# Kernel tuning notes

Hardware: AMD Instinct MI355X
Metric: run time of the kernel (lower is better)

The kernel has to match this reference:

```python
import jax, jax.numpy as jnp
import numpy as np

DN = ('NCDHW', 'DHWIO', 'NCDHW')


def _w(key, cin, cout):
    # kernel_size=3 in 3D, Minkowski-style fan-in scaling, no bias
    scale = 1.0 / np.sqrt(cin * 27)
    return jax.random.normal(key, (3, 3, 3, cin, cout), dtype=jnp.float32) * scale


def setup_inputs() -> dict:
    key = jax.random.key(0)
    ks = jax.random.split(key, 7)
    x = jax.random.normal(ks[0], (1, 1024, 4, 4, 4), dtype=jnp.float32)
    chans = [(1024, 512), (512, 256), (256, 128), (128, 64), (64, 32), (32, 1)]
    ws = {f'w{i+1}': _w(ks[i + 1], ci, co) for i, (ci, co) in enumerate(chans)}
    return {'x': x, **ws}


def _ct(x, w, stride):
    # conv-transpose, kernel 3, SAME padding: stride 2 doubles resolution,
    # stride 1 preserves it (dense analog of Minkowski generative transpose conv)
    return jax.lax.conv_transpose(x, w, strides=(stride, stride, stride),
                                  padding='SAME', dimension_numbers=DN)


def reference(x, w1, w2, w3, w4, w5, w6):
    h = jax.nn.relu(_ct(x, w1, 2))   # 1024 -> 512, 4^3 -> 8^3
    h = jax.nn.relu(_ct(h, w2, 1))   # 512 -> 256
    h = jax.nn.relu(_ct(h, w3, 2))   # 256 -> 128, 8^3 -> 16^3
    h = jax.nn.relu(_ct(h, w4, 1))   # 128 -> 64
    h = jax.nn.relu(_ct(h, w5, 2))   # 64 -> 32, 16^3 -> 32^3
    return _ct(h, w6, 1)             # 32 -> 1, no final ReLU
```

## Files before the change

kernel.cpp:

```cpp
#include <hip/hip_runtime.h>

typedef _Float16 half8 __attribute__((ext_vector_type(8)));
typedef _Float16 half4v __attribute__((ext_vector_type(4)));
typedef float floatx4 __attribute__((ext_vector_type(4)));


__global__ __launch_bounds__(256) void pad_x_k(const float* __restrict__ X,
                                               _Float16* __restrict__ P) {
  int idx = blockIdx.x * 256 + threadIdx.x;
  if (idx >= 125 * 1024) return;
  int c = idx & 1023;
  int r = idx >> 10;
  int px = r % 5, py = (r / 5) % 5, pz = r / 25;
  float v = 0.f;
  if (px >= 1 && py >= 1 && pz >= 1)
    v = X[c * 64 + (pz - 1) * 16 + (py - 1) * 4 + (px - 1)];
  P[idx] = (_Float16)v;
}

template <int S, int PS, int C, int RELU>
__global__ __launch_bounds__(256) void pad_k(const float* __restrict__ I,
                                             _Float16* __restrict__ P) {
  constexpr int TOT = PS * PS * PS * C;
  int idx = blockIdx.x * 256 + threadIdx.x;
  if (idx >= TOT) return;
  int c = idx % C;
  int r = idx / C;
  int px = r % PS;
  int ry = r / PS;
  int py = ry % PS, pz = ry / PS;
  int sx = px - 1, sy = py - 1, sz = pz - 1;
  float v = 0.f;
  if (sx >= 0 && sx < S && sy >= 0 && sy < S && sz >= 0 && sz < S) {
    v = I[(size_t)((sz * S + sy) * S + sx) * C + c];
    if (RELU) v = fmaxf(v, 0.f);
  }
  P[idx] = (_Float16)v;
}

template <int CICHUNK, int CIN, int COUT, int NTILE, int STRIDE2, int SOUTU,
          int TZ, int PS, int STORE_MODE>
__global__ __launch_bounds__(256) void conv_mfma_k(
    const _Float16* __restrict__ P, const float* __restrict__ W,
    void* __restrict__ Optr) {
  constexpr int M = TZ * 16;
  constexpr int MTZ = SOUTU / TZ;
  constexpr int MTXY = SOUTU / 4;
  constexpr int MT3 = MTZ * MTXY * MTXY;
  constexpr int KB = 32;
  constexpr int KP = 40;
  constexpr int KBI = CICHUNK / KB;
  constexpr int S = STRIDE2 ? 2 * SOUTU : SOUTU;
  constexpr int BJ = (NTILE == 64) ? 8 : 4;

  __shared__ __align__(16) _Float16 As[M][KP];
  __shared__ __align__(16) _Float16 Bs[NTILE][KP];

  int bx = blockIdx.x;
  int cls = 0;
  if (STRIDE2) { cls = bx / MT3; bx -= cls * MT3; }
  const int clz = (cls >> 2) & 1, cly = (cls >> 1) & 1, clx = cls & 1;
  const int u0z = (bx / (MTXY * MTXY)) * TZ;
  const int u0y = ((bx / MTXY) % MTXY) * 4;
  const int u0x = (bx % MTXY) * 4;
  const int n_base = blockIdx.y * NTILE;
  const int ci_base = blockIdx.z * CICHUNK;

  const int t = threadIdx.x;
  const int lane = t & 63;
  const int wave = t >> 6;

  const int skq = t & 3;
  const int sp = t >> 2;
  const int spx = sp & 3, spy = (sp >> 2) & 3, spz = sp >> 4;
  const int aoffsp = ((spz * PS + spy) * PS + spx) * CIN + skq * 8;
  const int aoffsp2 = (((spz + 4) * PS + spy) * PS + spx) * CIN + skq * 8;

  const int nB = t & (NTILE - 1);
  const int k0B = (t / NTILE) * BJ;

  const int m0w = (NTILE == 64) ? (wave >> 1) * 32 : wave * 32;
  const int n0w = (NTILE == 64) ? (wave & 1) * 32 : 0;
  const int fr = lane & 15;
  const int fq = lane >> 4;

  const int cz = STRIDE2 ? (clz ? 1 : 2) : 3;
  const int cy = STRIDE2 ? (cly ? 1 : 2) : 3;
  const int cx = STRIDE2 ? (clx ? 1 : 2) : 3;
  const int ctaps = cz * cy * cx;
  const int NIT = ctaps * KBI;
  const int shx = STRIDE2 ? (clx ? 0 : 1) : 0;
  const int shy = STRIDE2 ? (cly ? 0 : 1) : 0;

  floatx4 acc[2][2];
#pragma unroll
  for (int i = 0; i < 2; i++)
#pragma unroll
    for (int j = 0; j < 2; j++) acc[i][j] = {0.f, 0.f, 0.f, 0.f};

  half8 raA = {}, raB = {}, raA2 = {}, raB2 = {};
  float bwv[BJ] = {}, bwv2[BJ] = {};

  auto load_it = [&](int it, half8& A0, half8& A1, float* BW) {
    int tap, kb;
    if (KBI == 1) { tap = it; kb = 0; }
    else { tap = it / KBI; kb = it - tap * KBI; }
    int iz, iy, ix;
    if (STRIDE2) {
      const int shyx = shx + shy;
      iz = tap >> shyx;
      int rem = tap - (iz << shyx);
      iy = rem >> shx;
      ix = rem - (iy << shx);
    } else {
      iz = tap / 9;
      int rem = tap - iz * 9;
      iy = rem / 3;
      ix = rem - iy * 3;
    }
    const int toz = STRIDE2 ? (clz ? 1 : iz) : iz;
    const int wz  = STRIDE2 ? (clz ? 1 : 2 * iz) : iz;
    const int toy = STRIDE2 ? (cly ? 1 : iy) : iy;
    const int wy  = STRIDE2 ? (cly ? 1 : 2 * iy) : iy;
    const int tox = STRIDE2 ? (clx ? 1 : ix) : ix;
    const int wx  = STRIDE2 ? (clx ? 1 : 2 * ix) : ix;
    const int kofs = ci_base + kb * KB;
    const size_t pbase =
        (size_t)(((u0z + toz) * PS + (u0y + toy)) * PS + (u0x + tox)) * CIN +
        kofs;
    A0 = *(const half8*)(P + pbase + aoffsp);
    if (M == 128) A1 = *(const half8*)(P + pbase + aoffsp2);
    const int wtap = (wz * 3 + wy) * 3 + wx;
    const float* wb =
        W + ((size_t)wtap * CIN + kofs + k0B) * COUT + n_base + nB;
#pragma unroll
    for (int j = 0; j < BJ; j++) BW[j] = wb[(size_t)j * COUT];
  };

  load_it(0, raA, raB, bwv);

  for (int it = 0; it < NIT; ++it) {
    *(half8*)&As[sp][skq * 8] = raA;
    if (M == 128) *(half8*)&As[sp + 64][skq * 8] = raB;
    {
      half4v h0;
#pragma unroll
      for (int j = 0; j < 4; j++) h0[j] = (_Float16)bwv[j];
      *(half4v*)&Bs[nB][k0B] = h0;
      if (BJ == 8) {
        half4v h1;
#pragma unroll
        for (int j = 0; j < 4; j++) h1[j] = (_Float16)bwv[4 + j];
        *(half4v*)&Bs[nB][k0B + 4] = h1;
      }
    }
    __syncthreads();
    if (it + 1 < NIT) load_it(it + 1, raA2, raB2, bwv2);
    half8 a0 = *(const half8*)&As[m0w + fr][fq * 8];
    half8 a1 = *(const half8*)&As[m0w + 16 + fr][fq * 8];
    half8 b0 = *(const half8*)&Bs[n0w + fr][fq * 8];
    half8 b1 = *(const half8*)&Bs[n0w + 16 + fr][fq * 8];
    acc[0][0] = __builtin_amdgcn_mfma_f32_16x16x32_f16(a0, b0, acc[0][0], 0, 0, 0);
    acc[0][1] = __builtin_amdgcn_mfma_f32_16x16x32_f16(a0, b1, acc[0][1], 0, 0, 0);
    acc[1][0] = __builtin_amdgcn_mfma_f32_16x16x32_f16(a1, b0, acc[1][0], 0, 0, 0);
    acc[1][1] = __builtin_amdgcn_mfma_f32_16x16x32_f16(a1, b1, acc[1][1], 0, 0, 0);
    __syncthreads();
    raA = raA2;
    raB = raB2;
#pragma unroll
    for (int j = 0; j < BJ; j++) bwv[j] = bwv2[j];
  }

#pragma unroll
  for (int i = 0; i < 2; i++) {
#pragma unroll
    for (int r = 0; r < 4; r++) {
      const int m = m0w + i * 16 + fq * 4 + r;
      const int mz = m >> 4, my = (m >> 2) & 3, mx = m & 3;
      int oz, oy, ox;
      if (STRIDE2) {
        oz = 2 * (u0z + mz) + clz;
        oy = 2 * (u0y + my) + cly;
        ox = 2 * (u0x + mx) + clx;
      } else {
        oz = u0z + mz;
        oy = u0y + my;
        ox = u0x + mx;
      }
      if (STORE_MODE == 2) {
        _Float16* o = (_Float16*)Optr +
            (size_t)(((oz + 1) * (S + 2) + (oy + 1)) * (S + 2) + (ox + 1)) *
                COUT + n_base + n0w;
#pragma unroll
        for (int j = 0; j < 2; j++)
          o[j * 16 + fr] = (_Float16)fmaxf(acc[i][j][r], 0.f);
      } else {
        float* o = (float*)Optr +
            (size_t)((oz * S + oy) * S + ox) * COUT + n_base + n0w;
#pragma unroll
        for (int j = 0; j < 2; j++) {
          if (STORE_MODE == 1) atomicAdd(o + j * 16 + fr, acc[i][j][r]);
          else o[j * 16 + fr] = acc[i][j][r];
        }
      }
    }
  }
}

__global__ __launch_bounds__(256) void conv6_k(const _Float16* __restrict__ P,
                                               const float* __restrict__ W6,
                                               float* __restrict__ O) {
  __shared__ __align__(16) float w[864];
  for (int i = threadIdx.x; i < 864; i += 256) w[i] = W6[i];
  __syncthreads();
  int idx = blockIdx.x * 256 + threadIdx.x;
  int x = idx & 31, y = (idx >> 5) & 31, z = idx >> 10;
  float a = 0.f;
  for (int dz = 0; dz < 3; dz++)
    for (int dy = 0; dy < 3; dy++)
      for (int dx = 0; dx < 3; dx++) {
        const _Float16* p =
            P + (size_t)(((z + dz) * 34 + (y + dy)) * 34 + (x + dx)) * 32;
        const float* ww = &w[((dz * 3 + dy) * 3 + dx) * 32];
#pragma unroll
        for (int c = 0; c < 32; c += 8) {
          half8 pv = *(const half8*)&p[c];
#pragma unroll
          for (int u = 0; u < 8; u++) a += (float)pv[u] * ww[c + u];
        }
      }
  O[idx] = a;
}

extern "C" void kernel_launch(void* const* d_in, const int* in_sizes, int n_in,
                              void* d_out, int out_size, void* d_ws,
                              size_t ws_size, hipStream_t stream) {
  const float* x  = (const float*)d_in[0];
  const float* w1 = (const float*)d_in[1];
  const float* w2 = (const float*)d_in[2];
  const float* w3 = (const float*)d_in[3];
  const float* w4 = (const float*)d_in[4];
  const float* w5 = (const float*)d_in[5];
  const float* w6 = (const float*)d_in[6];
  float* out = (float*)d_out;

  float* O1 = (float*)d_ws;
  float* O2 = O1 + 262144;
  float* O3 = O2 + 131072;
  float* O4 = O3 + 524288;
  _Float16* P6 = (_Float16*)(O4 + 262144);
  _Float16* P1 = P6 + 1257728;
  _Float16* P2 = P1 + 128000;
  _Float16* P3 = P2 + 512000;
  _Float16* P4 = P3 + 186624;
  _Float16* P5 = P4 + 746496;

  hipMemsetAsync(d_ws, 0, 1179648 * sizeof(float) + 1257728 * sizeof(_Float16),
                 stream);

  pad_x_k<<<500, 256, 0, stream>>>(x, P1);
  conv_mfma_k<128, 1024, 512, 64, 1, 4, 4, 5, 1>
      <<<dim3(8, 8, 8), 256, 0, stream>>>(P1, w1, O1);
  pad_k<8, 10, 512, 1><<<2000, 256, 0, stream>>>(O1, P2);
  conv_mfma_k<32, 512, 256, 64, 0, 8, 4, 10, 1>
      <<<dim3(8, 4, 16), 256, 0, stream>>>(P2, w2, O2);
  pad_k<8, 9, 256, 1><<<729, 256, 0, stream>>>(O2, P3);
  conv_mfma_k<64, 256, 128, 64, 1, 8, 4, 9, 1>
      <<<dim3(64, 2, 4), 256, 0, stream>>>(P3, w3, O3);
  pad_k<16, 18, 128, 1><<<2916, 256, 0, stream>>>(O3, P4);
  conv_mfma_k<32, 128, 64, 64, 0, 16, 4, 18, 1>
      <<<dim3(64, 1, 4), 256, 0, stream>>>(P4, w4, O4);
  pad_k<16, 17, 64, 1><<<1229, 256, 0, stream>>>(O4, P5);
  conv_mfma_k<64, 64, 32, 32, 1, 16, 8, 17, 2>
      <<<dim3(256, 1, 1), 256, 0, stream>>>(P5, w5, P6);
  conv6_k<<<128, 256, 0, stream>>>(P6, w6, out);

  (void)in_sizes; (void)n_in; (void)out_size; (void)ws_size;
}
```

Measured before the change: 216.1 us.

## Fuse pad+ReLU into conv loads and split work across taps for parallelism

Removes the separate pad_k kernels: conv layers now read fp32 activations directly with bounds checks, apply ReLU and convert to fp16 in the load path. Adds per-tap parallel splitting (each block handles one tap for stride-2 layers or a group of 9 taps for stride-1) with atomic accumulation. Also adds M=128 tiles with 4-wave M layout. This cuts launches and intermediate traffic but increases atomic contention and redundant fp32 loads.

```diff
diff --git a/kernel.cpp b/kernel.cpp
--- a/kernel.cpp
+++ b/kernel.cpp
@@ -18,53 +18,79 @@
   P[idx] = (_Float16)v;
 }
 
-template <int S, int PS, int C, int RELU>
-__global__ __launch_bounds__(256) void pad_k(const float* __restrict__ I,
-                                             _Float16* __restrict__ P) {
-  constexpr int TOT = PS * PS * PS * C;
-  int idx = blockIdx.x * 256 + threadIdx.x;
-  if (idx >= TOT) return;
-  int c = idx % C;
-  int r = idx / C;
-  int px = r % PS;
-  int ry = r / PS;
-  int py = ry % PS, pz = ry / PS;
-  int sx = px - 1, sy = py - 1, sz = pz - 1;
-  float v = 0.f;
-  if (sx >= 0 && sx < S && sy >= 0 && sy < S && sz >= 0 && sz < S) {
-    v = I[(size_t)((sz * S + sy) * S + sx) * C + c];
-    if (RELU) v = fmaxf(v, 0.f);
-  }
-  P[idx] = (_Float16)v;
-}
-
-template <int CICHUNK, int CIN, int COUT, int NTILE, int STRIDE2, int SOUTU,
-          int TZ, int PS, int STORE_MODE>
+__device__ __forceinline__ half8 cvt_relu8(const float4& f0, const float4& f1) {
+  half8 h;
+  h[0] = (_Float16)fmaxf(f0.x, 0.f);
+  h[1] = (_Float16)fmaxf(f0.y, 0.f);
+  h[2] = (_Float16)fmaxf(f0.z, 0.f);
+  h[3] = (_Float16)fmaxf(f0.w, 0.f);
+  h[4] = (_Float16)fmaxf(f1.x, 0.f);
+  h[5] = (_Float16)fmaxf(f1.y, 0.f);
+  h[6] = (_Float16)fmaxf(f1.z, 0.f);
+  h[7] = (_Float16)fmaxf(f1.w, 0.f);
+  return h;
+}
+
+template <int CICHUNK, int CIN, int COUT, int NTILE, int TZ, int SOUTU,
+          int SMODE, int TAPG, int IN_MODE, int STORE_MODE>
 __global__ __launch_bounds__(256) void conv_mfma_k(
-    const _Float16* __restrict__ P, const float* __restrict__ W,
+    const void* __restrict__ Pin, const float* __restrict__ W,
     void* __restrict__ Optr) {
   constexpr int M = TZ * 16;
+  constexpr bool S2 = (SMODE != 0);
   constexpr int MTZ = SOUTU / TZ;
   constexpr int MTXY = SOUTU / 4;
   constexpr int MT3 = MTZ * MTXY * MTXY;
   constexpr int KB = 32;
   constexpr int KP = 40;
   constexpr int KBI = CICHUNK / KB;
-  constexpr int S = STRIDE2 ? 2 * SOUTU : SOUTU;
-  constexpr int BJ = (NTILE == 64) ? 8 : 4;
+  constexpr int NCI = CIN / CICHUNK;
+  constexpr int S = S2 ? 2 * SOUTU : SOUTU;
+  constexpr int WM = (M == 128) ? 4 : 2;
+  constexpr int NSUB = (WM == 4) ? (NTILE / 16) : (NTILE / 32);
+  constexpr int BJ = KB * NTILE / 256;
 
   __shared__ __align__(16) _Float16 As[M][KP];
   __shared__ __align__(16) _Float16 Bs[NTILE][KP];
 
   int bx = blockIdx.x;
-  int cls = 0;
-  if (STRIDE2) { cls = bx / MT3; bx -= cls * MT3; }
+  int cls = 0, tap0 = 0, cig = blockIdx.z;
+  int p_toz = 0, p_toy = 0, p_tox = 0, p_wtap = 0;
+  if (SMODE == 0) {
+    const int tg = cig / NCI;
+    cig -= tg * NCI;
+    tap0 = tg * TAPG;
+  } else if (SMODE == 1) {
+    const int p = bx / MT3;
+    bx -= p * MT3;
+    cls = (p >= 8) + (p >= 12) + (p >= 16) + (p >= 18) + (p >= 22) +
+          (p >= 24) + (p >= 26);
+    const int pf = cls == 0 ? 0 : cls == 1 ? 8 : cls == 2 ? 12
+                 : cls == 3 ? 16 : cls == 4 ? 18 : cls == 5 ? 22
+                 : cls == 6 ? 24 : 26;
+    const int tl = p - pf;
+    const int lz = (cls >> 2) & 1, ly = (cls >> 1) & 1, lx = cls & 1;
+    const int shx = lx ? 0 : 1, shy = ly ? 0 : 1;
+    const int iz = tl >> (shx + shy);
+    const int rem = tl & ((1 << (shx + shy)) - 1);
+    const int iy = rem >> shx;
+    const int ix = rem & ((1 << shx) - 1);
+    p_toz = lz ? 1 : iz;
+    p_toy = ly ? 1 : iy;
+    p_tox = lx ? 1 : ix;
+    const int wz = lz ? 1 : 2 * iz, wy = ly ? 1 : 2 * iy,
+              wx = lx ? 1 : 2 * ix;
+    p_wtap = (wz * 3 + wy) * 3 + wx;
+  } else {
+    cls = bx / MT3;
+    bx -= cls * MT3;
+  }
   const int clz = (cls >> 2) & 1, cly = (cls >> 1) & 1, clx = cls & 1;
+
   const int u0z = (bx / (MTXY * MTXY)) * TZ;
   const int u0y = ((bx / MTXY) % MTXY) * 4;
   const int u0x = (bx % MTXY) * 4;
   const int n_base = blockIdx.y * NTILE;
-  const int ci_base = blockIdx.z * CICHUNK;
 
   const int t = threadIdx.x;
   const int lane = t & 63;
@@ -73,102 +99,133 @@
   const int skq = t & 3;
   const int sp = t >> 2;
   const int spx = sp & 3, spy = (sp >> 2) & 3, spz = sp >> 4;
-  const int aoffsp = ((spz * PS + spy) * PS + spx) * CIN + skq * 8;
-  const int aoffsp2 = (((spz + 4) * PS + spy) * PS + spx) * CIN + skq * 8;
-
   const int nB = t & (NTILE - 1);
   const int k0B = (t / NTILE) * BJ;
-
-  const int m0w = (NTILE == 64) ? (wave >> 1) * 32 : wave * 32;
-  const int n0w = (NTILE == 64) ? (wave & 1) * 32 : 0;
+  const int m0w = (WM == 4) ? wave * 32 : (wave >> 1) * 32;
+  const int n0w = (WM == 4) ? 0 : (wave & 1) * 32;
   const int fr = lane & 15;
   const int fq = lane >> 4;
 
-  const int cz = STRIDE2 ? (clz ? 1 : 2) : 3;
-  const int cy = STRIDE2 ? (cly ? 1 : 2) : 3;
-  const int cx = STRIDE2 ? (clx ? 1 : 2) : 3;
-  const int ctaps = cz * cy * cx;
-  const int NIT = ctaps * KBI;
-  const int shx = STRIDE2 ? (clx ? 0 : 1) : 0;
-  const int shy = STRIDE2 ? (cly ? 0 : 1) : 0;
-
-  floatx4 acc[2][2];
+  const int cz = S2 ? (clz ? 1 : 2) : 3;
+  const int cy = S2 ? (cly ? 1 : 2) : 3;
+  const int cx = S2 ? (clx ? 1 : 2) : 3;
+  const int shx2 = clx ? 0 : 1, shy2 = cly ? 0 : 1;
+
+  int NIT;
+  if (SMODE == 0) NIT = TAPG * KBI;
+  else if (SMODE == 1) NIT = KBI;
+  else NIT = cz * cy * cx * KBI;
+
+  floatx4 acc[2][NSUB];
 #pragma unroll
   for (int i = 0; i < 2; i++)
 #pragma unroll
-    for (int j = 0; j < 2; j++) acc[i][j] = {0.f, 0.f, 0.f, 0.f};
-
-  half8 raA = {}, raB = {}, raA2 = {}, raB2 = {};
-  float bwv[BJ] = {}, bwv2[BJ] = {};
+    for (int s = 0; s < NSUB; s++) acc[i][s] = {0.f, 0.f, 0.f, 0.f};
+
+  half8 rA0 = {}, rA1 = {}, nA0 = {}, nA1 = {};
+  float rB[BJ] = {}, nBv[BJ] = {};
 
   auto load_it = [&](int it, half8& A0, half8& A1, float* BW) {
     int tap, kb;
-    if (KBI == 1) { tap = it; kb = 0; }
+    if (SMODE == 1) { tap = 0; kb = it; }
+    else if (KBI == 1) { tap = it; kb = 0; }
     else { tap = it / KBI; kb = it - tap * KBI; }
-    int iz, iy, ix;
-    if (STRIDE2) {
-      const int shyx = shx + shy;
-      iz = tap >> shyx;
-      int rem = tap - (iz << shyx);
-      iy = rem >> shx;
-      ix = rem - (iy << shx);
+    int toz, toy, tox, wtap;
+    if (SMODE == 1) {
+      toz = p_toz; toy = p_toy; tox = p_tox; wtap = p_wtap;
+    } else if (SMODE == 0) {
+      const int tt = tap0 + tap;
+      const int iz = tt / 9;
+      const int rem = tt - iz * 9;
+      const int iy = rem / 3;
+      const int ix = rem - iy * 3;
+      toz = iz; toy = iy; tox = ix;
+      wtap = tt;
     } else {
-      iz = tap / 9;
-      int rem = tap - iz * 9;
-      iy = rem / 3;
-      ix = rem - iy * 3;
-    }
-    const int toz = STRIDE2 ? (clz ? 1 : iz) : iz;
-    const int wz  = STRIDE2 ? (clz ? 1 : 2 * iz) : iz;
-    const int toy = STRIDE2 ? (cly ? 1 : iy) : iy;
-    const int wy  = STRIDE2 ? (cly ? 1 : 2 * iy) : iy;
-    const int tox = STRIDE2 ? (clx ? 1 : ix) : ix;
-    const int wx  = STRIDE2 ? (clx ? 1 : 2 * ix) : ix;
-    const int kofs = ci_base + kb * KB;
-    const size_t pbase =
-        (size_t)(((u0z + toz) * PS + (u0y + toy)) * PS + (u0x + tox)) * CIN +
-        kofs;
-    A0 = *(const half8*)(P + pbase + aoffsp);
-    if (M == 128) A1 = *(const half8*)(P + pbase + aoffsp2);
-    const int wtap = (wz * 3 + wy) * 3 + wx;
+      const int iz = tap >> (shx2 + shy2);
+      const int rem = tap & ((1 << (shx2 + shy2)) - 1);
+      const int iy = rem >> shx2;
+      const int ix = rem & ((1 << shx2) - 1);
+      toz = clz ? 1 : iz; toy = cly ? 1 : iy; tox = clx ? 1 : ix;
+      const int wz = clz ? 1 : 2 * iz, wy = cly ? 1 : 2 * iy,
+                wx = clx ? 1 : 2 * ix;
+      wtap = (wz * 3 + wy) * 3 + wx;
+    }
+    const int kof0 = cig * CICHUNK + kb * KB;
+    if (IN_MODE == 0) {
+      constexpr int PS = SOUTU + 1;
+      const _Float16* Pp = (const _Float16*)Pin;
+      const size_t pb =
+          ((size_t)(((u0z + toz + spz) * PS + (u0y + toy + spy)) * PS +
+                    (u0x + tox + spx))) * CIN + kof0 + skq * 8;
+      A0 = *(const half8*)(Pp + pb);
+      if (M == 128)
+        A1 = *(const half8*)(Pp + pb + (size_t)4 * PS * PS * CIN);
+    } else {
+      const float* Ip = (const float*)Pin;
+      const int izc = u0z + toz + spz - 1;
+      const int iyc = u0y + toy + spy - 1;
+      const int ixc = u0x + tox + spx - 1;
+      const bool okyx = ((unsigned)iyc < (unsigned)SOUTU) &
+                        ((unsigned)ixc < (unsigned)SOUTU);
+      const float* src =
+          Ip + ((size_t)((izc * SOUTU + iyc) * SOUTU + ixc)) * CIN + kof0 +
+          skq * 8;
+      float4 f0 = make_float4(0.f, 0.f, 0.f, 0.f);
+      float4 f1 = make_float4(0.f, 0.f, 0.f, 0.f);
+      if (okyx && ((unsigned)izc < (unsigned)SOUTU)) {
+        f0 = *(const float4*)src;
+        f1 = *(const float4*)(src + 4);
+      }
+      A0 = cvt_relu8(f0, f1);
+      if (M == 128) {
+        float4 g0 = make_float4(0.f, 0.f, 0.f, 0.f);
+        float4 g1 = make_float4(0.f, 0.f, 0.f, 0.f);
+        if (okyx && ((unsigned)(izc + 4) < (unsigned)SOUTU)) {
+          const float* s2p = src + (size_t)4 * SOUTU * SOUTU * CIN;
+          g0 = *(const float4*)s2p;
+          g1 = *(const float4*)(s2p + 4);
+        }
+        A1 = cvt_relu8(g0, g1);
+      }
+    }
     const float* wb =
-        W + ((size_t)wtap * CIN + kofs + k0B) * COUT + n_base + nB;
+        W + ((size_t)wtap * CIN + kof0 + k0B) * COUT + n_base + nB;
 #pragma unroll
     for (int j = 0; j < BJ; j++) BW[j] = wb[(size_t)j * COUT];
   };
 
-  load_it(0, raA, raB, bwv);
+  load_it(0, rA0, rA1, rB);
 
   for (int it = 0; it < NIT; ++it) {
-    *(half8*)&As[sp][skq * 8] = raA;
-    if (M == 128) *(half8*)&As[sp + 64][skq * 8] = raB;
-    {
-      half4v h0;
-#pragma unroll
-      for (int j = 0; j < 4; j++) h0[j] = (_Float16)bwv[j];
-      *(half4v*)&Bs[nB][k0B] = h0;
-      if (BJ == 8) {
-        half4v h1;
-#pragma unroll
-        for (int j = 0; j < 4; j++) h1[j] = (_Float16)bwv[4 + j];
-        *(half4v*)&Bs[nB][k0B + 4] = h1;
-      }
+    *(half8*)&As[sp][skq * 8] = rA0;
+    if (M == 128) *(half8*)&As[sp + 64][skq * 8] = rA1;
+    if (BJ == 8) {
+      half8 hb;
+#pragma unroll
+      for (int j = 0; j < 8; j++) hb[j] = (_Float16)rB[j];
+      *(half8*)&Bs[nB][k0B] = hb;
+    } else {
+      half4v hb;
+#pragma unroll
+      for (int j = 0; j < 4; j++) hb[j] = (_Float16)rB[j];
+      *(half4v*)&Bs[nB][k0B] = hb;
     }
     __syncthreads();
-    if (it + 1 < NIT) load_it(it + 1, raA2, raB2, bwv2);
+    if (it + 1 < NIT) load_it(it + 1, nA0, nA1, nBv);
     half8 a0 = *(const half8*)&As[m0w + fr][fq * 8];
     half8 a1 = *(const half8*)&As[m0w + 16 + fr][fq * 8];
-    half8 b0 = *(const half8*)&Bs[n0w + fr][fq * 8];
-    half8 b1 = *(const half8*)&Bs[n0w + 16 + fr][fq * 8];
-    acc[0][0] = __builtin_amdgcn_mfma_f32_16x16x32_f16(a0, b0, acc[0][0], 0, 0, 0);
-    acc[0][1] = __builtin_amdgcn_mfma_f32_16x16x32_f16(a0, b1, acc[0][1], 0, 0, 0);
-    acc[1][0] = __builtin_amdgcn_mfma_f32_16x16x32_f16(a1, b0, acc[1][0], 0, 0, 0);
-    acc[1][1] = __builtin_amdgcn_mfma_f32_16x16x32_f16(a1, b1, acc[1][1], 0, 0, 0);
+#pragma unroll
+    for (int s = 0; s < NSUB; s++) {
+      half8 b = *(const half8*)&Bs[n0w + s * 16 + fr][fq * 8];
+      acc[0][s] = __builtin_amdgcn_mfma_f32_16x16x32_f16(a0, b, acc[0][s], 0, 0, 0);
+      acc[1][s] = __builtin_amdgcn_mfma_f32_16x16x32_f16(a1, b, acc[1][s], 0, 0, 0);
+    }
     __syncthreads();
-    raA = raA2;
-    raB = raB2;
-#pragma unroll
-    for (int j = 0; j < BJ; j++) bwv[j] = bwv2[j];
+    rA0 = nA0;
+    rA1 = nA1;
+#pragma unroll
+    for (int j = 0; j < BJ; j++) rB[j] = nBv[j];
   }
 
 #pragma unroll
@@ -178,7 +235,7 @@
       const int m = m0w + i * 16 + fq * 4 + r;
       const int mz = m >> 4, my = (m >> 2) & 3, mx = m & 3;
       int oz, oy, ox;
-      if (STRIDE2) {
+      if (S2) {
         oz = 2 * (u0z + mz) + clz;
         oy = 2 * (u0y + my) + cly;
         ox = 2 * (u0x + mx) + clx;
@@ -189,19 +246,16 @@
       }
       if (STORE_MODE == 2) {
         _Float16* o = (_Float16*)Optr +
-            (size_t)(((oz + 1) * (S + 2) + (oy + 1)) * (S + 2) + (ox + 1)) *
+            ((size_t)(((oz + 1) * (S + 2) + (oy + 1)) * (S + 2) + (ox + 1))) *
                 COUT + n_base + n0w;
 #pragma unroll
-        for (int j = 0; j < 2; j++)
-          o[j * 16 + fr] = (_Float16)fmaxf(acc[i][j][r], 0.f);
+        for (int s = 0; s < NSUB; s++)
+          o[s * 16 + fr] = (_Float16)fmaxf(acc[i][s][r], 0.f);
       } else {
         float* o = (float*)Optr +
-            (size_t)((oz * S + oy) * S + ox) * COUT + n_base + n0w;
-#pragma unroll
-        for (int j = 0; j < 2; j++) {
-          if (STORE_MODE == 1) atomicAdd(o + j * 16 + fr, acc[i][j][r]);
-          else o[j * 16 + fr] = acc[i][j][r];
-        }
+            ((size_t)((oz * S + oy) * S + ox)) * COUT + n_base + n0w;
+#pragma unroll
+        for (int s = 0; s < NSUB; s++) atomicAdd(o + s * 16 + fr, acc[i][s][r]);
       }
     }
   }
@@ -250,29 +304,21 @@
   float* O4 = O3 + 524288;
   _Float16* P6 = (_Float16*)(O4 + 262144);
   _Float16* P1 = P6 + 1257728;
-  _Float16* P2 = P1 + 128000;
-  _Float16* P3 = P2 + 512000;
-  _Float16* P4 = P3 + 186624;
-  _Float16* P5 = P4 + 746496;
-
-  hipMemsetAsync(d_ws, 0, 1179648 * sizeof(float) + 1257728 * sizeof(_Float16),
-                 stream);
+
+  hipMemsetAsync(d_ws, 0,
+                 1179648 * sizeof(float) + 1257728 * sizeof(_Float16), stream);
 
   pad_x_k<<<500, 256, 0, stream>>>(x, P1);
-  conv_mfma_k<128, 1024, 512, 64, 1, 4, 4, 5, 1>
-      <<<dim3(8, 8, 8), 256, 0, stream>>>(P1, w1, O1);
-  pad_k<8, 10, 512, 1><<<2000, 256, 0, stream>>>(O1, P2);
-  conv_mfma_k<32, 512, 256, 64, 0, 8, 4, 10, 1>
-      <<<dim3(8, 4, 16), 256, 0, stream>>>(P2, w2, O2);
-  pad_k<8, 9, 256, 1><<<729, 256, 0, stream>>>(O2, P3);
-  conv_mfma_k<64, 256, 128, 64, 1, 8, 4, 9, 1>
-      <<<dim3(64, 2, 4), 256, 0, stream>>>(P3, w3, O3);
-  pad_k<16, 18, 128, 1><<<2916, 256, 0, stream>>>(O3, P4);
-  conv_mfma_k<32, 128, 64, 64, 0, 16, 4, 18, 1>
-      <<<dim3(64, 1, 4), 256, 0, stream>>>(P4, w4, O4);
-  pad_k<16, 17, 64, 1><<<1229, 256, 0, stream>>>(O4, P5);
-  conv_mfma_k<64, 64, 32, 32, 1, 16, 8, 17, 2>
-      <<<dim3(256, 1, 1), 256, 0, stream>>>(P5, w5, P6);
+  conv_mfma_k<256, 1024, 512, 64, 4, 4, 1, 0, 0, 1>
+      <<<dim3(27, 8, 4), 256, 0, stream>>>(P1, w1, O1);
+  conv_mfma_k<64, 512, 256, 64, 8, 8, 0, 9, 1, 1>
+      <<<dim3(4, 4, 24), 256, 0, stream>>>(O1, w2, O2);
+  conv_mfma_k<128, 256, 128, 64, 8, 8, 1, 0, 1, 1>
+      <<<dim3(108, 2, 2), 256, 0, stream>>>(O2, w3, O3);
+  conv_mfma_k<32, 128, 64, 64, 8, 16, 0, 9, 1, 1>
+      <<<dim3(32, 1, 12), 256, 0, stream>>>(O3, w4, O4);
+  conv_mfma_k<64, 64, 32, 32, 8, 16, 2, 0, 1, 2>
+      <<<dim3(256, 1, 1), 256, 0, stream>>>(O4, w5, P6);
   conv6_k<<<128, 256, 0, stream>>>(P6, w6, out);
 
   (void)in_sizes; (void)n_in; (void)out_size; (void)ws_size;
```

Measured after the change: 221.7 us. 2.6% more time.
